# Performance work log

Hardware: AMD Instinct MI355X
Metric: run time of the kernel (lower is better)

The kernel has to match this reference:

```python
import jax, jax.numpy as jnp
import numpy as np

HIDDEN = 100


def _mlp(x, w1, b1, w2, b2):
    # MLP(in, HIDDEN, output_size=out): Linear -> ReLU -> Linear
    return jnp.maximum(x @ w1 + b1, 0.0) @ w2 + b2


def _row_norm_mean(d):
    # mean_i sqrt(sum_j d_ij^2)  == torch.sqrt(einsum('ij,ij->i')).mean()
    return jnp.sqrt(jnp.einsum('ij,ij->i', d, d)).mean()


def _mismatch_1nn(mapped, target, idx):
    # torch_mapping_misclassified_1nn: cdist(mapped[idx], target), top-1 NN,
    # count non-integer distances at mismatched rows / len(idx).
    a = mapped[idx]                                     # [K, d]
    d2 = (jnp.sum(a * a, axis=1, keepdims=True)
          + jnp.sum(target * target, axis=1)[None, :]
          - 2.0 * a @ target.T)                         # [K, N]
    dist = jnp.sqrt(jnp.maximum(d2, 0.0))
    vals = jnp.min(dist, axis=1)                        # top-1 smallest value
    nn_inds = jnp.argmin(dist, axis=1)
    mismatch = (nn_inds != idx)
    count = (jnp.ceil(vals) - jnp.floor(vals)) * mismatch.astype(vals.dtype)
    return count.sum() / idx.shape[0]


def setup_inputs() -> dict:
    key = jax.random.key(0)
    ks = jax.random.split(key, 8)
    xN, yN, xd, yd, K = 25000, 25000, 100, 120, 8000
    s = 0.1
    return {
        'x_weight': jax.random.normal(ks[0], (xN, xd), jnp.float32) * s,
        'y_weight': jax.random.normal(ks[1], (yN, yd), jnp.float32) * s,
        'fx_w1': jax.random.normal(ks[2], (xd, HIDDEN), jnp.float32) * (1.0 / np.sqrt(xd)),
        'fx_b1': jnp.zeros((HIDDEN,), jnp.float32),
        'fx_w2': jax.random.normal(ks[3], (HIDDEN, yd), jnp.float32) * (1.0 / np.sqrt(HIDDEN)),
        'fx_b2': jnp.zeros((yd,), jnp.float32),
        'gy_w1': jax.random.normal(ks[4], (yd, HIDDEN), jnp.float32) * (1.0 / np.sqrt(yd)),
        'gy_b1': jnp.zeros((HIDDEN,), jnp.float32),
        'gy_w2': jax.random.normal(ks[5], (HIDDEN, xd), jnp.float32) * (1.0 / np.sqrt(HIDDEN)),
        'gy_b2': jnp.zeros((xd,), jnp.float32),
        'index_map': jax.random.randint(ks[6], (K, 2), 0, min(xN, yN), jnp.int64 if jax.config.jax_enable_x64 else jnp.int32),
    }


def reference(x_weight, y_weight, fx_w1, fx_b1, fx_w2, fx_b2,
              gy_w1, gy_b1, gy_w2, gy_b2, index_map):
    x_mapped = _mlp(x_weight, fx_w1, fx_b1, fx_w2, fx_b2)   # fx(x_emb)  [xN, yd]
    y_mapped = _mlp(y_weight, gy_w1, gy_b1, gy_w2, gy_b2)   # gy(y_emb)  [yN, xd]

    # cycle losses
    x_rt = _mlp(x_mapped, gy_w1, gy_b1, gy_w2, gy_b2)
    cycle_fx = _row_norm_mean(x_rt - x_weight)
    y_rt = _mlp(y_mapped, fx_w1, fx_b1, fx_w2, fx_b2)
    cycle_gy = _row_norm_mean(y_rt - y_weight)

    x_intersect = index_map[:, 0]
    y_intersect = index_map[:, 1]

    # supervised alignment losses
    sup_x = _row_norm_mean(x_mapped[x_intersect] - y_weight[y_intersect])
    sup_y = _row_norm_mean(y_mapped[y_intersect] - x_weight[x_intersect])

    # 1-NN mismatch losses (the cdist + top-1 hot spots)
    fx_mismatch = _mismatch_1nn(x_mapped, y_weight, x_intersect)
    gy_mismatch = _mismatch_1nn(y_mapped, x_weight, y_intersect)

    return cycle_fx + cycle_gy + sup_x + fx_mismatch + sup_y + gy_mismatch
```

## Files before the change

### kernel.cpp

```cpp
#include <hip/hip_runtime.h>
#include <hip/hip_bf16.h>
#include <math.h>

#define HIDDEN 100

typedef __attribute__((ext_vector_type(8))) short bf16x8;
typedef __attribute__((ext_vector_type(4))) float f32x4;

__device__ inline unsigned short f2bf(float v) {
    union { float f; unsigned u; } x; x.f = v;
    unsigned r = x.u + 0x7fff + ((x.u >> 16) & 1);
    return (unsigned short)(r >> 16);
}

constexpr int NPTS  = 25000;
constexpr int KPAIR = 8000;
constexpr int NC    = 28;
constexpr int CHUNK = 896;
constexpr int NPAD  = NC * CHUNK;
constexpr int HS    = 136;
constexpr int NB_SUP = 2000;
constexpr int GM     = (NPTS + 31) / 32;
constexpr int NB_MLP = 2 * GM;
constexpr int PREP_B8 = (2 * NPAD) / 8;

__global__ __launch_bounds__(256) void w_prep(
    const float* __restrict__ W1, unsigned short* __restrict__ P1,
    const float* __restrict__ W2, unsigned short* __restrict__ P2,
    const float* __restrict__ W3, unsigned short* __restrict__ P3,
    const float* __restrict__ W4, unsigned short* __restrict__ P4)
{
    const int ln = threadIdx.x & 63;
    int b = blockIdx.x * 4 + (threadIdx.x >> 6);
    if (b >= 116) return;
    const float* W; unsigned short* P; int DK, DN, NT;
    if (b < 28)      {          W = W1; P = P1; DK = 100; DN = 100; NT = 7; }
    else if (b < 60) { b -= 28; W = W2; P = P2; DK = 100; DN = 120; NT = 8; }
    else if (b < 88) { b -= 60; W = W3; P = P3; DK = 120; DN = 100; NT = 7; }
    else             { b -= 88; W = W4; P = P4; DK = 100; DN = 100; NT = 7; }
    const int kt = b / NT, nt = b - kt * NT;
    const int n  = nt * 16 + (ln & 15);
    const int k0 = kt * 32 + (ln >> 4) * 8;
    unsigned short* dst = P + ((size_t)(kt * NT + nt) * 64 + ln) * 8;
    #pragma unroll
    for (int j = 0; j < 8; j++) {
        const int k = k0 + j;
        const float f = (k < DK && n < DN) ? W[k * DN + n] : 0.f;
        dst[j] = f2bf(f);
    }
}

template<int NT>
__device__ inline void run_stage(const bf16x8 af[4], const unsigned short* __restrict__ WP,
                                 int ln, f32x4 acc[NT])
{
    #pragma unroll
    for (int nt = 0; nt < NT; nt++) acc[nt] = (f32x4){0.f, 0.f, 0.f, 0.f};
    #pragma unroll
    for (int kt = 0; kt < 4; kt++) {
        #pragma unroll
        for (int nt = 0; nt < NT; nt++) {
            const bf16x8 wf = *reinterpret_cast<const bf16x8*>(WP + ((size_t)(kt * NT + nt) * 64 + ln) * 8);
            acc[nt] = __builtin_amdgcn_mfma_f32_16x16x32_bf16(af[kt], wf, acc[nt], 0, 0, 0);
        }
    }
}

template<int NT, int DN, bool RELU>
__device__ inline void pack_h(const f32x4 acc[NT], const float* __restrict__ B,
                              unsigned short* __restrict__ Hs, int col, int quad)
{
    #pragma unroll
    for (int nt = 0; nt < NT; nt++) {
        const int n = nt * 16 + col;
        const float b = (n < DN) ? B[n] : 0.f;
        #pragma unroll
        for (int r = 0; r < 4; r++) {
            float v = acc[nt][r] + b;
            if (RELU) v = fmaxf(v, 0.f);
            Hs[(quad * 4 + r) * HS + n] = f2bf(v);
        }
    }
}

template<int NT, int DN>
__device__ inline void store_pack(const f32x4 acc[NT], const float* __restrict__ B,
                                  float* __restrict__ Y, unsigned short* __restrict__ Hs,
                                  int rowbase, int col, int quad, int N)
{
    #pragma unroll
    for (int nt = 0; nt < NT; nt++) {
        const int n = nt * 16 + col;
        const float b = (n < DN) ? B[n] : 0.f;
        #pragma unroll
        for (int r = 0; r < 4; r++) {
            const float v = acc[nt][r] + b;
            const int row = rowbase + quad * 4 + r;
            if (n < DN && row < N) Y[(size_t)row * DN + n] = v;
            Hs[(quad * 4 + r) * HS + n] = f2bf(v);
        }
    }
}

__device__ inline void load_haf(const unsigned short* __restrict__ Hs, int col, int quad,
                                bf16x8 af[4])
{
    const unsigned short* p = Hs + col * HS + quad * 8;
    #pragma unroll
    for (int kt = 0; kt < 4; kt++)
        af[kt] = *reinterpret_cast<const bf16x8*>(p + kt * 32);
}

template<int DIN>
__device__ inline void load_a_direct(const float* __restrict__ X, int r, int quad,
                                     bf16x8 af[4])
{
    const float* ap = X + (size_t)r * DIN;
    #pragma unroll
    for (int kt = 0; kt < 4; kt++) {
        const int base = kt * 32 + quad * 8;
        float4 v0, v1;
        if (DIN == 100) {
            if (base == 96) {
                v0 = *reinterpret_cast<const float4*>(ap + 96);
                v1 = make_float4(0.f, 0.f, 0.f, 0.f);
            } else {
                const int b = (base < 92) ? base : 92;
                v0 = *reinterpret_cast<const float4*>(ap + b);
                v1 = *reinterpret_cast<const float4*>(ap + b + 4);
            }
        } else {
            const int b = (base < 112) ? base : 112;
            v0 = *reinterpret_cast<const float4*>(ap + b);
            v1 = *reinterpret_cast<const float4*>(ap + b + 4);
        }
        bf16x8 f;
        f[0] = (short)f2bf(v0.x); f[1] = (short)f2bf(v0.y);
        f[2] = (short)f2bf(v0.z); f[3] = (short)f2bf(v0.w);
        f[4] = (short)f2bf(v1.x); f[5] = (short)f2bf(v1.y);
        f[6] = (short)f2bf(v1.z); f[7] = (short)f2bf(v1.w);
        af[kt] = f;
    }
}

template<int NT, int DN>
__device__ inline float norm_stage(const f32x4 acc[NT], const float* __restrict__ B,
                                   const float* __restrict__ REF,
                                   int rowbase, int col, int quad, int N)
{
    float ra[4] = {0.f, 0.f, 0.f, 0.f};
    #pragma unroll
    for (int nt = 0; nt < NT; nt++) {
        const int n = nt * 16 + col;
        if (n < DN) {
            const float b = B[n];
            #pragma unroll
            for (int r = 0; r < 4; r++) {
                const int row = rowbase + quad * 4 + r;
                if (row < N) {
                    const float d = acc[nt][r] + b - REF[(size_t)row * DN + n];
                    ra[r] = fmaf(d, d, ra[r]);
                }
            }
        }
    }
    #pragma unroll
    for (int o = 1; o < 16; o <<= 1) {
        #pragma unroll
        for (int r = 0; r < 4; r++) ra[r] += __shfl_xor(ra[r], o);
    }
    float s = 0.f;
    if (col == 0) {
        #pragma unroll
        for (int r = 0; r < 4; r++)
            if (rowbase + quad * 4 + r < N) s += sqrtf(ra[r]);
    }
    return s;
}

template<int DIN, int DMID, int NT2, int NTF>
__device__ __forceinline__ void mlp_chain(
    int bid,
    const float* __restrict__ XREF,
    const unsigned short* __restrict__ WP1, const float* __restrict__ B1,
    const unsigned short* __restrict__ WP2, const float* __restrict__ B2,
    const unsigned short* __restrict__ WP3, const float* __restrict__ B3,
    const unsigned short* __restrict__ WP4, const float* __restrict__ B4,
    float* __restrict__ Y, float* __restrict__ part, int N,
    unsigned short (*H)[16 * HS], float* bred)
{
    const int tid = threadIdx.x;
    const int wv = tid >> 6, ln = tid & 63;
    const int col = ln & 15, quad = ln >> 4;
    const int rowbase = bid * 32 + wv * 16;

    {
        unsigned* Hz = reinterpret_cast<unsigned*>(H[wv]);
        for (int i = ln; i < 16 * HS / 2; i += 64) Hz[i] = 0u;
    }

    bf16x8 af[4];
    load_a_direct<DIN>(XREF, min(rowbase + col, N - 1), quad, af);

    f32x4 accA[7];
    run_stage<7>(af, WP1, ln, accA);
    pack_h<7, HIDDEN, true>(accA, B1, H[wv], col, quad);
    load_haf(H[wv], col, quad, af);

    f32x4 accB[NT2];
    run_stage<NT2>(af, WP2, ln, accB);
    store_pack<NT2, DMID>(accB, B2, Y, H[wv], rowbase, col, quad, N);
    load_haf(H[wv], col, quad, af);

    run_stage<7>(af, WP3, ln, accA);
    pack_h<7, HIDDEN, true>(accA, B3, H[wv], col, quad);
    load_haf(H[wv], col, quad, af);

    f32x4 accC[NTF];
    run_stage<NTF>(af, WP4, ln, accC);
    const float s = norm_stage<NTF, DIN>(accC, B4, XREF, rowbase, col, quad, N);

    if (col == 0) bred[wv * 4 + quad] = s;
    __syncthreads();
    if (tid == 0) {
        float t = 0.f;
        #pragma unroll
        for (int i = 0; i < 8; i++) t += bred[i];
        part[bid] = t;
    }
}

__global__ __launch_bounds__(128) void mlp_prep(
    const float* __restrict__ xw, const float* __restrict__ yw,
    unsigned short* __restrict__ ybf, unsigned short* __restrict__ xbf,
    const unsigned short* __restrict__ wp_fx1, const float* __restrict__ fx_b1,
    const unsigned short* __restrict__ wp_fx2, const float* __restrict__ fx_b2,
    const unsigned short* __restrict__ wp_gy1, const float* __restrict__ gy_b1,
    const unsigned short* __restrict__ wp_gy2, const float* __restrict__ gy_b2,
    float* __restrict__ xm, float* __restrict__ ym,
    float* __restrict__ part, int N)
{
    __shared__ unsigned short H[2][16 * HS];
    __shared__ float bred[8];

    if (blockIdx.x < GM) {
        mlp_chain<100, 120, 8, 7>(blockIdx.x, xw,
            wp_fx1, fx_b1, wp_fx2, fx_b2, wp_gy1, gy_b1, wp_gy2, gy_b2,
            xm, part, N, H, bred);
        return;
    }
    if (blockIdx.x < 2 * GM) {
        mlp_chain<120, 100, 7, 8>(blockIdx.x - GM, yw,
            wp_gy1, gy_b1, wp_gy2, gy_b2, wp_fx1, fx_b1, wp_fx2, fx_b2,
            ym, part + GM, N, H, bred);
        return;
    }

    const int bid = blockIdx.x - 2 * GM;
    const int wv = threadIdx.x >> 6, ln = threadIdx.x & 63;
    #pragma unroll
    for (int i = 0; i < 4; i++) {
        const int gw = bid * 8 + wv * 4 + i;
        const int isY = (gw < NPAD);
        const int r = isY ? gw : gw - NPAD;
        const int D = isY ? 120 : 100;
        unsigned short* dst = (isY ? ybf : xbf) + (size_t)r * 128;
        if (r < N) {
            const float* src = (isY ? yw : xw) + (size_t)r * D;
            const float v0 = (ln < D) ? src[ln] : 0.f;
            const float v1 = (ln + 64 < D) ? src[ln + 64] : 0.f;
            float s = fmaf(v0, v0, v1 * v1);
            #pragma unroll
            for (int o = 1; o < 64; o <<= 1) s += __shfl_xor(s, o);
            dst[ln] = f2bf(v0);
            dst[ln + 64] = (ln == 63) ? f2bf(s) : f2bf(v1);
        } else {
            dst[ln] = 0;
            dst[ln + 64] = (ln == 63) ? f2bf(1e30f) : (unsigned short)0;
        }
    }
}

__global__ __launch_bounds__(256) void sup_gather(
    const float* __restrict__ xm, const float* __restrict__ ym,
    const float* __restrict__ xw, const float* __restrict__ yw,
    const int* __restrict__ im, int K, float* __restrict__ part,
    unsigned short* __restrict__ axf, unsigned short* __restrict__ ayf)
{
    const int gw = (int)((blockIdx.x * 256 + threadIdx.x) >> 6);
    const int ln = threadIdx.x & 63;
    const int wv = threadIdx.x >> 6;
    float cnt = 0.f;
    if (gw < K) {
        const int xi = im[2 * gw], yi = im[2 * gw + 1];
        const float* a = xm + (size_t)xi * 120;
        const float* b = yw + (size_t)yi * 120;
        const float a0 = a[ln];
        const float a1 = (ln + 64 < 120) ? a[ln + 64] : 0.f;
        float s1 = 0.f;
        { const float d0 = a0 - b[ln]; s1 = d0 * d0; }
        if (ln + 64 < 120) { const float d1 = a1 - b[ln + 64]; s1 = fmaf(d1, d1, s1); }
        unsigned short* pax = axf + (size_t)gw * 128;
        pax[ln] = f2bf(-2.f * a0);
        pax[ln + 64] = (ln == 63) ? f2bf(1.f) : ((ln + 64 < 120) ? f2bf(-2.f * a1) : (unsigned short)0);

        const float* c = ym + (size_t)yi * 100;
        const float* e = xw + (size_t)xi * 100;
        const float c0 = c[ln];
        const float c1 = (ln + 64 < 100) ? c[ln + 64] : 0.f;
        float s2 = 0.f;
        { const float d0 = c0 - e[ln]; s2 = d0 * d0; }
        if (ln + 64 < 100) { const float d1 = c1 - e[ln + 64]; s2 = fmaf(d1, d1, s2); }
        unsigned short* pay = ayf + (size_t)gw * 128;
        pay[ln] = f2bf(-2.f * c0);
        pay[ln + 64] = (ln == 63) ? f2bf(1.f) : ((ln + 64 < 100) ? f2bf(-2.f * c1) : (unsigned short)0);

        #pragma unroll
        for (int o = 32; o > 0; o >>= 1) { s1 += __shfl_down(s1, o); s2 += __shfl_down(s2, o); }
        if (ln == 0) cnt = sqrtf(s1) + sqrtf(s2);
    }
    __shared__ float wsum[4];
    if (ln == 0) wsum[wv] = cnt;
    __syncthreads();
    if (threadIdx.x == 0)
        part[blockIdx.x] = wsum[0] + wsum[1] + wsum[2] + wsum[3];
}

__device__ inline void stage32(const unsigned short* __restrict__ T, int jbase,
                               unsigned char* dst0, int wv, int ln)
{
    #pragma unroll
    for (int h = 0; h < 2; h++) {
        const int c = h * 256 + wv * 64 + ln;
        const int r = c >> 4;
        const int gc = (c & 15) ^ (r & 15);
        const unsigned short* g = T + ((size_t)(jbase + r) << 7) + gc * 8;
        unsigned char* l = dst0 + h * 4096 + wv * 1024;
        __builtin_amdgcn_global_load_lds(
            (const __attribute__((address_space(1))) void*)g,
            (__attribute__((address_space(3))) void*)l, 16, 0, 0);
    }
}

__global__ __launch_bounds__(256, 3) void nn_mfma(
    const unsigned short* __restrict__ A0, const unsigned short* __restrict__ T0,
    float* __restrict__ pm0, int* __restrict__ pi0,
    const unsigned short* __restrict__ A1, const unsigned short* __restrict__ T1,
    float* __restrict__ pm1, int* __restrict__ pi1,
    int K)
{
    __shared__ __align__(16) unsigned char smem[32768];
    float (*rm)[64][17] = reinterpret_cast<float(*)[64][17]>(smem);

    const unsigned short* A = blockIdx.z ? A1 : A0;
    const unsigned short* T = blockIdx.z ? T1 : T0;
    float* pmin = blockIdx.z ? pm1 : pm0;
    int*   pidx = blockIdx.z ? pi1 : pi0;

    const int tid = threadIdx.x;
    const int wv = tid >> 6, ln = tid & 63;
    const int col = ln & 15, quad = ln >> 4;
    const int k0 = blockIdx.x * 256;
    const int jstart = blockIdx.y * CHUNK;
    constexpr int NSTEPS = CHUNK / 64;

    bf16x8 afrag[4][4];
    #pragma unroll
    for (int t = 0; t < 4; t++) {
        const int ar = min(k0 + wv * 64 + t * 16 + col, K - 1);
        const unsigned short* ab = A + (size_t)ar * 128 + quad * 8;
        #pragma unroll
        for (int s = 0; s < 4; s++)
            afrag[t][s] = *reinterpret_cast<const bf16x8*>(ab + s * 32);
    }

    float m[4][4];
    #pragma unroll
    for (int t = 0; t < 4; t++)
        #pragma unroll
        for (int r = 0; r < 4; r++) m[t][r] = __builtin_inff();

    stage32(T, jstart,      smem,        wv, ln);
    stage32(T, jstart + 32, smem + 8192, wv, ln);
    __syncthreads();

    for (int ti = 0; ti < NSTEPS; ti++) {
        const int cur = ti & 1;
        if (ti + 1 < NSTEPS) {
            const int jn = jstart + (ti + 1) * 64;
            stage32(T, jn,      smem + (cur ^ 1) * 16384,        wv, ln);
            stage32(T, jn + 32, smem + (cur ^ 1) * 16384 + 8192, wv, ln);
        }

        #pragma unroll
        for (int h = 0; h < 2; h++) {
            const unsigned short* base = (const unsigned short*)(smem + cur * 16384 + h * 8192);
            const unsigned lowbase = (unsigned)((jstart + ti * 64 + h * 32) >> 4);
            #pragma unroll
            for (int sub = 0; sub < 2; sub++) {
                bf16x8 bfr[4];
                const int rr = sub * 16 + col;
                #pragma unroll
                for (int s = 0; s < 4; s++) {
                    const int ch = rr * 16 + ((quad + s * 4) ^ col);
                    bfr[s] = *reinterpret_cast<const bf16x8*>(base + ch * 8);
                }
                const unsigned low = lowbase + sub;
                #pragma unroll
                for (int t = 0; t < 4; t++) {
                    f32x4 acc = {0.f, 0.f, 0.f, 0.f};
                    #pragma unroll
                    for (int s = 0; s < 4; s++)
                        acc = __builtin_amdgcn_mfma_f32_16x16x32_bf16(afrag[t][s], bfr[s], acc, 0, 0, 0);
                    #pragma unroll
                    for (int r = 0; r < 4; r++) {
                        const unsigned u = (__float_as_uint(acc[r]) & 0xFFFFF800u) | low;
                        m[t][r] = fminf(m[t][r], __uint_as_float(u));
                    }
                }
            }
        }
        __syncthreads();
    }

    #pragma unroll
    for (int t = 0; t < 4; t++)
        #pragma unroll
        for (int r = 0; r < 4; r++)
            rm[wv][t * 16 + quad * 4 + r][col] = m[t][r];
    __syncthreads();

    const int k = k0 + tid;
    if (k < K) {
        const int w = tid >> 6, rr = tid & 63;
        float best = rm[w][rr][0];
        int bc = 0;
        #pragma unroll
        for (int c = 1; c < 16; c++) {
            const float v = rm[w][rr][c];
            if (v < best) { best = v; bc = c; }
        }
        const int j = (int)(((__float_as_uint(best) & 0x7FFu) << 4) | (unsigned)bc);
        pmin[(size_t)k * NC + blockIdx.y] = best;
        pidx[(size_t)k * NC + blockIdx.y] = j;
    }
}

__global__ __launch_bounds__(256) void finish_all(
    const int* __restrict__ im,
    const float* __restrict__ pm0, const int* __restrict__ pi0,
    const float* __restrict__ pm1, const int* __restrict__ pi1,
    const float* __restrict__ part_sup, const float* __restrict__ part_mlp,
    int K, float* __restrict__ out, float inv_k, float inv_n)
{
    const int gid = blockIdx.x * 256 + threadIdx.x;
    const int stride = gridDim.x * 256;
    float local = 0.f;

    for (int p = gid; p < 2 * K; p += stride) {
        const int dir = (p >= K);
        const int kk = dir ? p - K : p;
        const float* pm = dir ? pm1 : pm0;
        const int*   pi = dir ? pi1 : pi0;
        float best = __builtin_inff();
        int bi = 0x7fffffff;
        #pragma unroll
        for (int c = 0; c < NC; c++) {
            const float v = pm[(size_t)kk * NC + c];
            const int  ii = pi[(size_t)kk * NC + c];
            if (v < best || (v == best && ii < bi)) { best = v; bi = ii; }
        }
        if (bi != im[2 * kk + dir]) local += inv_k;
    }
    for (int i = gid; i < NB_SUP; i += stride) local += part_sup[i] * inv_k;
    for (int i = gid; i < NB_MLP; i += stride) local += part_mlp[i] * inv_n;

    #pragma unroll
    for (int o = 32; o > 0; o >>= 1) local += __shfl_down(local, o);
    __shared__ float wsum[4];
    if ((threadIdx.x & 63) == 0) wsum[threadIdx.x >> 6] = local;
    __syncthreads();
    if (threadIdx.x == 0) {
        const float t = wsum[0] + wsum[1] + wsum[2] + wsum[3];
        if (t != 0.f) atomicAdd(out, t);
    }
}

extern "C" void kernel_launch(void* const* d_in, const int* in_sizes, int n_in,
                              void* d_out, int out_size, void* d_ws, size_t ws_size,
                              hipStream_t stream)
{
    const float* xw    = (const float*)d_in[0];
    const float* yw    = (const float*)d_in[1];
    const float* fx_w1 = (const float*)d_in[2];
    const float* fx_b1 = (const float*)d_in[3];
    const float* fx_w2 = (const float*)d_in[4];
    const float* fx_b2 = (const float*)d_in[5];
    const float* gy_w1 = (const float*)d_in[6];
    const float* gy_b1 = (const float*)d_in[7];
    const float* gy_w2 = (const float*)d_in[8];
    const float* gy_b2 = (const float*)d_in[9];
    const int*   imap  = (const int*)d_in[10];
    float* out = (float*)d_out;
    float* ws  = (float*)d_ws;

    constexpr int N = NPTS, K = KPAIR;

    float* xm      = ws;
    float* ym      = xm + (size_t)N * 120;
    float* pmin_fx = ym + (size_t)N * 100;
    int*   pidx_fx = (int*)(pmin_fx + (size_t)K * NC);
    float* pmin_gy = (float*)(pidx_fx + (size_t)K * NC);
    int*   pidx_gy = (int*)(pmin_gy + (size_t)K * NC);
    unsigned short* ybf = (unsigned short*)(pidx_gy + (size_t)K * NC);
    unsigned short* xbf = ybf + (size_t)NPAD * 128;
    unsigned short* axf = xbf + (size_t)NPAD * 128;
    unsigned short* ayf = axf + (size_t)K * 128;
    unsigned short* wp_fx1 = ayf + (size_t)K * 128;
    unsigned short* wp_fx2 = wp_fx1 + 28 * 512;
    unsigned short* wp_gy1 = wp_fx2 + 32 * 512;
    unsigned short* wp_gy2 = wp_gy1 + 28 * 512;
    float* part_sup = (float*)(wp_gy2 + 28 * 512);
    float* part_mlp = part_sup + NB_SUP;

    hipMemsetAsync(d_out, 0, sizeof(float), stream);

    w_prep<<<29, 256, 0, stream>>>(fx_w1, wp_fx1, fx_w2, wp_fx2,
                                   gy_w1, wp_gy1, gy_w2, wp_gy2);

    mlp_prep<<<2 * GM + PREP_B8, 128, 0, stream>>>(
        xw, yw, ybf, xbf,
        wp_fx1, fx_b1, wp_fx2, fx_b2, wp_gy1, gy_b1, wp_gy2, gy_b2,
        xm, ym, part_mlp, N);

    sup_gather<<<NB_SUP, 256, 0, stream>>>(xm, ym, xw, yw, imap, K, part_sup, axf, ayf);

    dim3 g1((K + 255) / 256, NC, 2);
    nn_mfma<<<g1, 256, 0, stream>>>(axf, ybf, pmin_fx, pidx_fx,
                                    ayf, xbf, pmin_gy, pidx_gy, K);

    finish_all<<<64, 256, 0, stream>>>(
        imap, pmin_fx, pidx_fx, pmin_gy, pidx_gy, part_sup, part_mlp,
        K, out, 1.f / K, 1.f / N);
}
```

Before: 226.3 us.

## Switch nearest-neighbor distance GEMM from bf16 to fp8 scaled MFMA

The 1-NN distance kernel now stores query and target embeddings as fp8 and uses the 16x16x128 f8f6f4 scaled MFMA, so one instruction replaces four bf16 MFMAs per tile and the bytes staged into LDS are halved. Target squared norms move out of the packed row into a separate fp32 array that is added after the MFMA. The target prep pass moves out of the MLP kernel and merges with weight packing into one launch. The cost is much coarser fp8 precision on the distances, which can change the argmin and the ceil/floor count compared with the reference.

```diff
diff --git a/kernel.cpp b/kernel.cpp
--- a/kernel.cpp
+++ b/kernel.cpp
@@ -5,12 +5,17 @@
 #define HIDDEN 100
 
 typedef __attribute__((ext_vector_type(8))) short bf16x8;
+typedef __attribute__((ext_vector_type(8))) int   i32x8;
 typedef __attribute__((ext_vector_type(4))) float f32x4;
 
 __device__ inline unsigned short f2bf(float v) {
     union { float f; unsigned u; } x; x.f = v;
     unsigned r = x.u + 0x7fff + ((x.u >> 16) & 1);
     return (unsigned short)(r >> 16);
+}
+
+__device__ inline unsigned char f2fp8(float v) {
+    return (unsigned char)(__builtin_amdgcn_cvt_pk_fp8_f32(v, 0.f, 0, false) & 0xFF);
 }
 
 constexpr int NPTS  = 25000;
@@ -22,16 +27,46 @@
 constexpr int NB_SUP = 2000;
 constexpr int GM     = (NPTS + 31) / 32;
 constexpr int NB_MLP = 2 * GM;
-constexpr int PREP_B8 = (2 * NPAD) / 8;
-
-__global__ __launch_bounds__(256) void w_prep(
+constexpr int PREP_B = (2 * NPAD) / 16;
+
+__global__ __launch_bounds__(256) void prep_kernel(
+    const float* __restrict__ YW, unsigned char* __restrict__ ybf8, float* __restrict__ tny,
+    const float* __restrict__ XW, unsigned char* __restrict__ xbf8, float* __restrict__ tnx,
     const float* __restrict__ W1, unsigned short* __restrict__ P1,
     const float* __restrict__ W2, unsigned short* __restrict__ P2,
     const float* __restrict__ W3, unsigned short* __restrict__ P3,
-    const float* __restrict__ W4, unsigned short* __restrict__ P4)
+    const float* __restrict__ W4, unsigned short* __restrict__ P4,
+    int N)
 {
     const int ln = threadIdx.x & 63;
-    int b = blockIdx.x * 4 + (threadIdx.x >> 6);
+    if (blockIdx.x < PREP_B) {
+        const int g0 = blockIdx.x * 16 + (threadIdx.x >> 6) * 4;
+        #pragma unroll
+        for (int i = 0; i < 4; i++) {
+            const int gw = g0 + i;
+            const int isY = (gw < NPAD);
+            const int r = isY ? gw : gw - NPAD;
+            const int D = isY ? 120 : 100;
+            unsigned char* dst = (isY ? ybf8 : xbf8) + (size_t)r * 128;
+            if (r < N) {
+                const float* src = (isY ? YW : XW) + (size_t)r * D;
+                const float v0 = (ln < D) ? src[ln] : 0.f;
+                const float v1 = (ln + 64 < D) ? src[ln + 64] : 0.f;
+                float s = fmaf(v0, v0, v1 * v1);
+                #pragma unroll
+                for (int o = 1; o < 64; o <<= 1) s += __shfl_xor(s, o);
+                if (ln == 0) (isY ? tny : tnx)[r] = s;
+                dst[ln] = f2fp8(v0);
+                dst[ln + 64] = f2fp8(v1);
+            } else {
+                dst[ln] = 0;
+                dst[ln + 64] = 0;
+                if (ln == 0) (isY ? tny : tnx)[r] = 1e30f;
+            }
+        }
+        return;
+    }
+    int b = (blockIdx.x - PREP_B) * 4 + (threadIdx.x >> 6);
     if (b >= 116) return;
     const float* W; unsigned short* P; int DK, DN, NT;
     if (b < 28)      {          W = W1; P = P1; DK = 100; DN = 100; NT = 7; }
@@ -230,9 +265,8 @@
     }
 }
 
-__global__ __launch_bounds__(128) void mlp_prep(
+__global__ __launch_bounds__(128) void mlp_both(
     const float* __restrict__ xw, const float* __restrict__ yw,
-    unsigned short* __restrict__ ybf, unsigned short* __restrict__ xbf,
     const unsigned short* __restrict__ wp_fx1, const float* __restrict__ fx_b1,
     const unsigned short* __restrict__ wp_fx2, const float* __restrict__ fx_b2,
     const unsigned short* __restrict__ wp_gy1, const float* __restrict__ gy_b1,
@@ -242,42 +276,14 @@
 {
     __shared__ unsigned short H[2][16 * HS];
     __shared__ float bred[8];
-
     if (blockIdx.x < GM) {
         mlp_chain<100, 120, 8, 7>(blockIdx.x, xw,
             wp_fx1, fx_b1, wp_fx2, fx_b2, wp_gy1, gy_b1, wp_gy2, gy_b2,
             xm, part, N, H, bred);
-        return;
-    }
-    if (blockIdx.x < 2 * GM) {
+    } else {
         mlp_chain<120, 100, 7, 8>(blockIdx.x - GM, yw,
             wp_gy1, gy_b1, wp_gy2, gy_b2, wp_fx1, fx_b1, wp_fx2, fx_b2,
             ym, part + GM, N, H, bred);
-        return;
-    }
-
-    const int bid = blockIdx.x - 2 * GM;
-    const int wv = threadIdx.x >> 6, ln = threadIdx.x & 63;
-    #pragma unroll
-    for (int i = 0; i < 4; i++) {
-        const int gw = bid * 8 + wv * 4 + i;
-        const int isY = (gw < NPAD);
-        const int r = isY ? gw : gw - NPAD;
-        const int D = isY ? 120 : 100;
-        unsigned short* dst = (isY ? ybf : xbf) + (size_t)r * 128;
-        if (r < N) {
-            const float* src = (isY ? yw : xw) + (size_t)r * D;
-            const float v0 = (ln < D) ? src[ln] : 0.f;
-            const float v1 = (ln + 64 < D) ? src[ln + 64] : 0.f;
-            float s = fmaf(v0, v0, v1 * v1);
-            #pragma unroll
-            for (int o = 1; o < 64; o <<= 1) s += __shfl_xor(s, o);
-            dst[ln] = f2bf(v0);
-            dst[ln + 64] = (ln == 63) ? f2bf(s) : f2bf(v1);
-        } else {
-            dst[ln] = 0;
-            dst[ln + 64] = (ln == 63) ? f2bf(1e30f) : (unsigned short)0;
-        }
     }
 }
 
@@ -285,7 +291,7 @@
     const float* __restrict__ xm, const float* __restrict__ ym,
     const float* __restrict__ xw, const float* __restrict__ yw,
     const int* __restrict__ im, int K, float* __restrict__ part,
-    unsigned short* __restrict__ axf, unsigned short* __restrict__ ayf)
+    unsigned char* __restrict__ axf8, unsigned char* __restrict__ ayf8)
 {
     const int gw = (int)((blockIdx.x * 256 + threadIdx.x) >> 6);
     const int ln = threadIdx.x & 63;
@@ -300,9 +306,9 @@
         float s1 = 0.f;
         { const float d0 = a0 - b[ln]; s1 = d0 * d0; }
         if (ln + 64 < 120) { const float d1 = a1 - b[ln + 64]; s1 = fmaf(d1, d1, s1); }
-        unsigned short* pax = axf + (size_t)gw * 128;
-        pax[ln] = f2bf(-2.f * a0);
-        pax[ln + 64] = (ln == 63) ? f2bf(1.f) : ((ln + 64 < 120) ? f2bf(-2.f * a1) : (unsigned short)0);
+        unsigned char* pax = axf8 + (size_t)gw * 128;
+        pax[ln] = f2fp8(-2.f * a0);
+        pax[ln + 64] = f2fp8(-2.f * a1);
 
         const float* c = ym + (size_t)yi * 100;
         const float* e = xw + (size_t)xi * 100;
@@ -311,9 +317,9 @@
         float s2 = 0.f;
         { const float d0 = c0 - e[ln]; s2 = d0 * d0; }
         if (ln + 64 < 100) { const float d1 = c1 - e[ln + 64]; s2 = fmaf(d1, d1, s2); }
-        unsigned short* pay = ayf + (size_t)gw * 128;
-        pay[ln] = f2bf(-2.f * c0);
-        pay[ln + 64] = (ln == 63) ? f2bf(1.f) : ((ln + 64 < 100) ? f2bf(-2.f * c1) : (unsigned short)0);
+        unsigned char* pay = ayf8 + (size_t)gw * 128;
+        pay[ln] = f2fp8(-2.f * c0);
+        pay[ln + 64] = f2fp8(-2.f * c1);
 
         #pragma unroll
         for (int o = 32; o > 0; o >>= 1) { s1 += __shfl_down(s1, o); s2 += __shfl_down(s2, o); }
@@ -326,34 +332,32 @@
         part[blockIdx.x] = wsum[0] + wsum[1] + wsum[2] + wsum[3];
 }
 
-__device__ inline void stage32(const unsigned short* __restrict__ T, int jbase,
-                               unsigned char* dst0, int wv, int ln)
-{
-    #pragma unroll
-    for (int h = 0; h < 2; h++) {
-        const int c = h * 256 + wv * 64 + ln;
-        const int r = c >> 4;
-        const int gc = (c & 15) ^ (r & 15);
-        const unsigned short* g = T + ((size_t)(jbase + r) << 7) + gc * 8;
-        unsigned char* l = dst0 + h * 4096 + wv * 1024;
-        __builtin_amdgcn_global_load_lds(
-            (const __attribute__((address_space(1))) void*)g,
-            (__attribute__((address_space(3))) void*)l, 16, 0, 0);
-    }
+__device__ inline void stage32f8(const unsigned char* __restrict__ T, int jbase,
+                                 unsigned char* dst0, int wv, int ln)
+{
+    const int c = wv * 64 + ln;
+    const int r = c >> 3;
+    const int gc = (c & 7) ^ (r & 7);
+    const unsigned char* g = T + ((size_t)(jbase + r) << 7) + gc * 16;
+    unsigned char* l = dst0 + wv * 1024 + ln * 16;
+    __builtin_amdgcn_global_load_lds(
+        (const __attribute__((address_space(1))) void*)g,
+        (__attribute__((address_space(3))) void*)l, 16, 0, 0);
 }
 
 __global__ __launch_bounds__(256, 3) void nn_mfma(
-    const unsigned short* __restrict__ A0, const unsigned short* __restrict__ T0,
-    float* __restrict__ pm0, int* __restrict__ pi0,
-    const unsigned short* __restrict__ A1, const unsigned short* __restrict__ T1,
-    float* __restrict__ pm1, int* __restrict__ pi1,
+    const unsigned char* __restrict__ A0, const unsigned char* __restrict__ T0,
+    const float* __restrict__ TN0, float* __restrict__ pm0, int* __restrict__ pi0,
+    const unsigned char* __restrict__ A1, const unsigned char* __restrict__ T1,
+    const float* __restrict__ TN1, float* __restrict__ pm1, int* __restrict__ pi1,
     int K)
 {
-    __shared__ __align__(16) unsigned char smem[32768];
+    __shared__ __align__(16) unsigned char smem[17408];
     float (*rm)[64][17] = reinterpret_cast<float(*)[64][17]>(smem);
 
-    const unsigned short* A = blockIdx.z ? A1 : A0;
-    const unsigned short* T = blockIdx.z ? T1 : T0;
+    const unsigned char* A = blockIdx.z ? A1 : A0;
+    const unsigned char* T = blockIdx.z ? T1 : T0;
+    const float* TN = blockIdx.z ? TN1 : TN0;
     float* pmin = blockIdx.z ? pm1 : pm0;
     int*   pidx = blockIdx.z ? pi1 : pi0;
 
@@ -364,14 +368,14 @@
     const int jstart = blockIdx.y * CHUNK;
     constexpr int NSTEPS = CHUNK / 64;
 
-    bf16x8 afrag[4][4];
+    i32x8 afrag[4];
     #pragma unroll
     for (int t = 0; t < 4; t++) {
         const int ar = min(k0 + wv * 64 + t * 16 + col, K - 1);
-        const unsigned short* ab = A + (size_t)ar * 128 + quad * 8;
-        #pragma unroll
-        for (int s = 0; s < 4; s++)
-            afrag[t][s] = *reinterpret_cast<const bf16x8*>(ab + s * 32);
+        const uint4* ab = reinterpret_cast<const uint4*>(A + (size_t)ar * 128 + quad * 32);
+        const uint4 lo = ab[0], hi = ab[1];
+        afrag[t] = (i32x8){(int)lo.x, (int)lo.y, (int)lo.z, (int)lo.w,
+                           (int)hi.x, (int)hi.y, (int)hi.z, (int)hi.w};
     }
 
     float m[4][4];
@@ -380,41 +384,49 @@
         #pragma unroll
         for (int r = 0; r < 4; r++) m[t][r] = __builtin_inff();
 
-    stage32(T, jstart,      smem,        wv, ln);
-    stage32(T, jstart + 32, smem + 8192, wv, ln);
+    stage32f8(T, jstart,      smem,        wv, ln);
+    stage32f8(T, jstart + 32, smem + 4096, wv, ln);
     __syncthreads();
 
     for (int ti = 0; ti < NSTEPS; ti++) {
         const int cur = ti & 1;
+        const int jbase = jstart + ti * 64;
         if (ti + 1 < NSTEPS) {
-            const int jn = jstart + (ti + 1) * 64;
-            stage32(T, jn,      smem + (cur ^ 1) * 16384,        wv, ln);
-            stage32(T, jn + 32, smem + (cur ^ 1) * 16384 + 8192, wv, ln);
-        }
+            stage32f8(T, jbase + 64, smem + (cur ^ 1) * 8192,        wv, ln);
+            stage32f8(T, jbase + 96, smem + (cur ^ 1) * 8192 + 4096, wv, ln);
+        }
+
+        float tnv[2][2];
+        #pragma unroll
+        for (int h = 0; h < 2; h++)
+            #pragma unroll
+            for (int sub = 0; sub < 2; sub++)
+                tnv[h][sub] = TN[jbase + h * 32 + sub * 16 + col];
 
         #pragma unroll
         for (int h = 0; h < 2; h++) {
-            const unsigned short* base = (const unsigned short*)(smem + cur * 16384 + h * 8192);
-            const unsigned lowbase = (unsigned)((jstart + ti * 64 + h * 32) >> 4);
+            const unsigned char* base = smem + cur * 8192 + h * 4096;
+            const unsigned lowbase = (unsigned)((jbase + h * 32) >> 4);
             #pragma unroll
             for (int sub = 0; sub < 2; sub++) {
-                bf16x8 bfr[4];
-                const int rr = sub * 16 + col;
-                #pragma unroll
-                for (int s = 0; s < 4; s++) {
-                    const int ch = rr * 16 + ((quad + s * 4) ^ col);
-                    bfr[s] = *reinterpret_cast<const bf16x8*>(base + ch * 8);
-                }
+                const int rT = sub * 16 + col;
+                const uint4 lo = *reinterpret_cast<const uint4*>(
+                    base + (rT * 8 + ((2 * quad + 0) ^ (rT & 7))) * 16);
+                const uint4 hi = *reinterpret_cast<const uint4*>(
+                    base + (rT * 8 + ((2 * quad + 1) ^ (rT & 7))) * 16);
+                const i32x8 bfr = (i32x8){(int)lo.x, (int)lo.y, (int)lo.z, (int)lo.w,
+                                          (int)hi.x, (int)hi.y, (int)hi.z, (int)hi.w};
                 const unsigned low = lowbase + sub;
+                const float tval = tnv[h][sub];
                 #pragma unroll
                 for (int t = 0; t < 4; t++) {
                     f32x4 acc = {0.f, 0.f, 0.f, 0.f};
-                    #pragma unroll
-                    for (int s = 0; s < 4; s++)
-                        acc = __builtin_amdgcn_mfma_f32_16x16x32_bf16(afrag[t][s], bfr[s], acc, 0, 0, 0);
+                    acc = __builtin_amdgcn_mfma_scale_f32_16x16x128_f8f6f4(
+                        afrag[t], bfr, acc, 0, 0, 0, 0x7F7F7F7F, 0, 0x7F7F7F7F);
                     #pragma unroll
                     for (int r = 0; r < 4; r++) {
-                        const unsigned u = (__float_as_uint(acc[r]) & 0xFFFFF800u) | low;
+                        const float val = acc[r] + tval;
+                        const unsigned u = (__float_as_uint(val) & 0xFFFFF800u) | low;
                         m[t][r] = fminf(m[t][r], __uint_as_float(u));
                     }
                 }
@@ -508,15 +520,17 @@
 
     float* xm      = ws;
     float* ym      = xm + (size_t)N * 120;
-    float* pmin_fx = ym + (size_t)N * 100;
+    float* tn_y    = ym + (size_t)N * 100;
+    float* tn_x    = tn_y + NPAD;
+    float* pmin_fx = tn_x + NPAD;
     int*   pidx_fx = (int*)(pmin_fx + (size_t)K * NC);
     float* pmin_gy = (float*)(pidx_fx + (size_t)K * NC);
     int*   pidx_gy = (int*)(pmin_gy + (size_t)K * NC);
-    unsigned short* ybf = (unsigned short*)(pidx_gy + (size_t)K * NC);
-    unsigned short* xbf = ybf + (size_t)NPAD * 128;
-    unsigned short* axf = xbf + (size_t)NPAD * 128;
-    unsigned short* ayf = axf + (size_t)K * 128;
-    unsigned short* wp_fx1 = ayf + (size_t)K * 128;
+    unsigned char* ybf8 = (unsigned char*)(pidx_gy + (size_t)K * NC);
+    unsigned char* xbf8 = ybf8 + (size_t)NPAD * 128;
+    unsigned char* axf8 = xbf8 + (size_t)NPAD * 128;
+    unsigned char* ayf8 = axf8 + (size_t)K * 128;
+    unsigned short* wp_fx1 = (unsigned short*)(ayf8 + (size_t)K * 128);
     unsigned short* wp_fx2 = wp_fx1 + 28 * 512;
     unsigned short* wp_gy1 = wp_fx2 + 32 * 512;
     unsigned short* wp_gy2 = wp_gy1 + 28 * 512;
@@ -525,19 +539,20 @@
 
     hipMemsetAsync(d_out, 0, sizeof(float), stream);
 
-    w_prep<<<29, 256, 0, stream>>>(fx_w1, wp_fx1, fx_w2, wp_fx2,
-                                   gy_w1, wp_gy1, gy_w2, wp_gy2);
-
-    mlp_prep<<<2 * GM + PREP_B8, 128, 0, stream>>>(
-        xw, yw, ybf, xbf,
+    prep_kernel<<<PREP_B + 29, 256, 0, stream>>>(
+        yw, ybf8, tn_y, xw, xbf8, tn_x,
+        fx_w1, wp_fx1, fx_w2, wp_fx2, gy_w1, wp_gy1, gy_w2, wp_gy2, N);
+
+    mlp_both<<<2 * GM, 128, 0, stream>>>(
+        xw, yw,
         wp_fx1, fx_b1, wp_fx2, fx_b2, wp_gy1, gy_b1, wp_gy2, gy_b2,
         xm, ym, part_mlp, N);
 
-    sup_gather<<<NB_SUP, 256, 0, stream>>>(xm, ym, xw, yw, imap, K, part_sup, axf, ayf);
+    sup_gather<<<NB_SUP, 256, 0, stream>>>(xm, ym, xw, yw, imap, K, part_sup, axf8, ayf8);
 
     dim3 g1((K + 255) / 256, NC, 2);
-    nn_mfma<<<g1, 256, 0, stream>>>(axf, ybf, pmin_fx, pidx_fx,
-                                    ayf, xbf, pmin_gy, pidx_gy, K);
+    nn_mfma<<<g1, 256, 0, stream>>>(axf8, ybf8, tn_y, pmin_fx, pidx_fx,
+                                    ayf8, xbf8, tn_x, pmin_gy, pidx_gy, K);
 
     finish_all<<<64, 256, 0, stream>>>(
         imap, pmin_fx, pidx_fx, pmin_gy, pidx_gy, part_sup, part_mlp,
```

New measurement: 199.0 us. -12.1%, faster.
